# Performance work log

Measured on AMD Instinct MI355X. Metric: run time of the kernel, lower is better.

## Reference

```python
import jax, jax.numpy as jnp
import numpy as np

L = 14  # max_relative_position
H = 12  # num_heads
HD = 64  # head_dim


def rel_pos_embed(N, table_v, table_h):
    # 2D relative-position embedding with a leading CLS token (index 0).
    n = N - 1
    s = int(n ** 0.5)  # grid side (14)
    r = jnp.arange(n)
    dv = r[None, :] // s - r[:, None] // s  # vertical distance
    dh = r[None, :] % s - r[:, None] % s   # horizontal distance
    iv = jnp.clip(dv, -L, L) + L + 1
    ih = jnp.clip(dh, -L, L) + L + 1
    iv = jnp.pad(iv, ((1, 0), (1, 0)))  # CLS row/col -> index 0
    ih = jnp.pad(ih, ((1, 0), (1, 0)))
    return table_v[iv] + table_h[ih]  # [N, N, HD]


def setup_inputs() -> dict:
    key = jax.random.key(0)
    ks = jax.random.split(key, 11)
    B, N, E = 64, 197, 768
    T = 2 * L + 2  # rel-pos table rows (30)
    std = 0.02
    return {
        "x": jax.random.normal(ks[0], (B, N, E), jnp.float32),
        "wq": jax.random.normal(ks[1], (E, H * HD), jnp.float32) * std,
        "wk": jax.random.normal(ks[2], (E, H * HD), jnp.float32) * std,
        "wv": jax.random.normal(ks[3], (E, H * HD), jnp.float32) * std,
        "wproj": jax.random.normal(ks[4], (H * HD, E), jnp.float32) * std,
        "bproj": jnp.zeros((E,), jnp.float32),
        "rk_v": jax.random.normal(ks[5], (T, HD), jnp.float32) * std,
        "rk_h": jax.random.normal(ks[6], (T, HD), jnp.float32) * std,
        "rv_v": jax.random.normal(ks[7], (T, HD), jnp.float32) * std,
        "rv_h": jax.random.normal(ks[8], (T, HD), jnp.float32) * std,
    }


def reference(x, wq, wk, wv, wproj, bproj, rk_v, rk_h, rv_v, rv_h):
    B, N, E = x.shape
    scale = HD ** -0.5
    q = (x @ wq).reshape(B, N, H, HD).transpose(0, 2, 1, 3)  # [B,H,N,HD]
    k = (x @ wk).reshape(B, N, H, HD).transpose(0, 2, 1, 3)
    v = (x @ wv).reshape(B, N, H, HD).transpose(0, 2, 1, 3)

    attn = jnp.einsum('bhid,bhjd->bhij', q, k) * scale
    rpk = rel_pos_embed(N, rk_v, rk_h)  # [N,N,HD]
    attn = attn + jnp.einsum('bhid,ijd->bhij', q, rpk) * scale
    attn = jax.nn.softmax(attn, axis=-1)

    out = jnp.einsum('bhij,bhjd->bhid', attn, v)
    rpv = rel_pos_embed(N, rv_v, rv_h)
    out = out + jnp.einsum('bhij,ijd->bhid', attn, rpv)

    out = out.transpose(0, 2, 1, 3).reshape(B, N, H * HD)
    return out @ wproj + bproj
```

## Files before the change

### kernel.cpp

```cpp
#include <hip/hip_runtime.h>
#include <math.h>

typedef _Float16 f16;
typedef __attribute__((ext_vector_type(8))) _Float16 f16x8;
typedef __attribute__((ext_vector_type(4))) _Float16 f16x4;
typedef __attribute__((ext_vector_type(4))) float f32x4;

#define NH 12
#define HDIM 64
#define NTOK 197
#define EDIM 768
#define NB 64
#define MROWS (NB*NTOK)

__device__ __forceinline__ void wfence() {
    asm volatile("s_waitcnt lgkmcnt(0)" ::: "memory");
    __builtin_amdgcn_sched_barrier(0);
    __builtin_amdgcn_wave_barrier();
}

__device__ __forceinline__ unsigned div14(unsigned n) { return (n * 4682u) >> 16; }

__device__ __forceinline__ void gload16(const f16* g, f16* lds_base) {
    __builtin_amdgcn_global_load_lds(
        (const __attribute__((address_space(1))) void*)g,
        (__attribute__((address_space(3))) void*)lds_base, 16, 0, 0);
}

__global__ __launch_bounds__(256) void convert_x(
    const float* __restrict__ x, f16* __restrict__ xh)
{
    int idx = blockIdx.x * 256 + threadIdx.x;
    const float4* s = (const float4*)x + (size_t)idx * 2;
    float4 a = s[0], b = s[1];
    f16x8 h;
    h[0]=(f16)a.x; h[1]=(f16)a.y; h[2]=(f16)a.z; h[3]=(f16)a.w;
    h[4]=(f16)b.x; h[5]=(f16)b.y; h[6]=(f16)b.z; h[7]=(f16)b.w;
    *(f16x8*)(xh + (size_t)idx * 8) = h;
}

__global__ __launch_bounds__(256) void transpose_w(
    const float* __restrict__ wq, const float* __restrict__ wk,
    const float* __restrict__ wv, const float* __restrict__ wp,
    f16* __restrict__ wqkvT, f16* __restrict__ wpT)
{
    __shared__ float T[64][65];
    int m = blockIdx.z;
    const float* src = (m==0)?wq:(m==1)?wk:(m==2)?wv:wp;
    int k0 = blockIdx.x * 64, n0 = blockIdx.y * 64;
    int cidx = threadIdx.x & 63, r4 = threadIdx.x >> 6;
#pragma unroll
    for (int rr = 0; rr < 16; ++rr) {
        int kl = rr*4 + r4;
        T[kl][cidx] = src[(size_t)(k0+kl)*EDIM + n0 + cidx];
    }
    __syncthreads();
    f16* dst = (m < 3) ? (wqkvT + (size_t)m*EDIM*EDIM) : wpT;
#pragma unroll
    for (int rr = 0; rr < 16; ++rr) {
        int nl = rr*4 + r4;
        dst[(size_t)(n0+nl)*EDIM + k0 + cidx] = (f16)T[cidx][nl];
    }
}

__global__ __launch_bounds__(256) void prep_static(
    const float* __restrict__ rkv, const float* __restrict__ rkh,
    f16* __restrict__ gA, f16* __restrict__ gt_buf)
{
    int t = blockIdx.x * 256 + threadIdx.x;
    int stride = gridDim.x * 256;
    for (int i = t; i < 272*104; i += stride) {
        int row = i / 104, c = i - row*104;
        f16 v = (f16)0.f;
        if (c < 64) {
            if (row >= 208 && row < 238)      v = (f16)rkv[(row-208)*64 + c];
            else if (row >= 240 && row < 270) v = (f16)rkh[(row-240)*64 + c];
        } else if (c < 96 && row < 208) {
            int g = c - 64;
            if (row == 0) { if (g == 14 || g == 30) v = (f16)1.f; }
            else if (row <= 196) {
                int rm = row - 1;
                int gv = (int)div14((unsigned)rm), gh = rm - gv*14;
                if (g == gv || g == 16 + gh) v = (f16)1.f;
            }
        }
        gA[i] = v;
    }
    for (int i = t; i < 32*232; i += stride) {
        int g = i / 232, j = i - g*232;
        f16 v = (f16)0.f;
        if (j >= 1 && j <= 196) {
            int jm = j - 1;
            int gv = (int)div14((unsigned)jm), gh = jm - gv*14;
            if ((g < 14 && gv == g) || (g >= 16 && g < 30 && gh == g - 16))
                v = (f16)1.f;
        }
        gt_buf[i] = v;
    }
}

__global__ __launch_bounds__(512, 2) void gemm256(
    const f16* __restrict__ A, const f16* __restrict__ Bt,
    f16* __restrict__ q_o, f16* __restrict__ k_o, f16* __restrict__ v_o,
    float* __restrict__ p_o, const float* __restrict__ bias, int mode, int nxb)
{
    __shared__ f16 lds[4*16384];

    const int tid = threadIdx.x;
    const int l = tid & 63, w = tid >> 6;
    const int lr = l & 15, lq = l >> 4;
    const int wr = w >> 2, wc = w & 3;

    const int nwg = gridDim.x, orig = blockIdx.x;
    const int xcd = orig & 7, qc = nwg >> 3, rc = nwg & 7;
    const int wgid = (xcd < rc ? xcd*(qc+1) : rc*(qc+1) + (xcd-rc)*qc) + (orig >> 3);
    const int mband = wgid / nxb, nband = wgid - mband*nxb;
    const int m0 = mband << 8, n0 = nband << 8;

    const int scol = (((tid & 7) ^ ((tid >> 3) & 7)) << 3);
    const f16* aG[4]; const f16* bG[4];
#pragma unroll
    for (int p = 0; p < 4; ++p) {
        int rt = p*64 + (tid >> 3);
        int ra = m0 + rt; if (ra >= MROWS) ra = MROWS - 1;
        aG[p] = A  + (size_t)ra * EDIM + scol;
        bG[p] = Bt + (size_t)(n0 + rt) * EDIM + scol;
    }
    const int lbase = w * 512;

    f32x4 acc[8][4];
#pragma unroll
    for (int mt = 0; mt < 8; ++mt)
#pragma unroll
        for (int nt = 0; nt < 4; ++nt) {
            acc[mt][nt][0]=0.f; acc[mt][nt][1]=0.f;
            acc[mt][nt][2]=0.f; acc[mt][nt][3]=0.f;
        }

#pragma unroll
    for (int p = 0; p < 4; ++p) {
        gload16(aG[p], &lds[p*4096 + lbase]);
        gload16(bG[p], &lds[32768 + p*4096 + lbase]);
    }
    asm volatile("s_waitcnt vmcnt(0)" ::: "memory");
    __builtin_amdgcn_sched_barrier(0);
    __builtin_amdgcn_s_barrier();

    const int swz = (lr & 7) << 3;
    int cur = 0;
    for (int kt = 0; kt < 12; ++kt) {
        if (kt < 11) {
            const int ko = (kt + 1) * 64;
            const int nb = (cur ^ 1) * 16384;
#pragma unroll
            for (int p = 0; p < 4; ++p) {
                gload16(aG[p] + ko, &lds[nb + p*4096 + lbase]);
                gload16(bG[p] + ko, &lds[32768 + nb + p*4096 + lbase]);
            }
        }
        __builtin_amdgcn_sched_barrier(0);
        const f16* Ab = &lds[cur * 16384];
        const f16* Bb = &lds[32768 + cur * 16384];
#pragma unroll
        for (int ks = 0; ks < 2; ++ks) {
            const int kb = (ks*32 + lq*8) ^ swz;
            f16x8 bf[4];
#pragma unroll
            for (int nt = 0; nt < 4; ++nt)
                bf[nt] = *(const f16x8*)&Bb[(wc*64 + nt*16 + lr)*64 + kb];
#pragma unroll
            for (int mt = 0; mt < 8; ++mt) {
                f16x8 af = *(const f16x8*)&Ab[(wr*128 + mt*16 + lr)*64 + kb];
#pragma unroll
                for (int nt = 0; nt < 4; ++nt)
                    acc[mt][nt] = __builtin_amdgcn_mfma_f32_16x16x32_f16(
                        af, bf[nt], acc[mt][nt], 0, 0, 0);
            }
        }
        asm volatile("s_waitcnt vmcnt(0)" ::: "memory");
        __builtin_amdgcn_sched_barrier(0);
        __builtin_amdgcn_s_barrier();
        cur ^= 1;
    }

    if (mode == 0) {
        const int mat   = n0 / EDIM;
        const int hbase = ((n0 % EDIM) >> 6) + wc;
        f16* dst = (mat == 0) ? q_o : (mat == 1) ? k_o : v_o;
        f16* scr = &lds[w * 2304];
#pragma unroll
        for (int mt2 = 0; mt2 < 4; ++mt2) {
#pragma unroll
            for (int mtp = 0; mtp < 2; ++mtp) {
                const int mt = mt2*2 + mtp;
#pragma unroll
                for (int nt = 0; nt < 4; ++nt)
#pragma unroll
                    for (int rg = 0; rg < 4; ++rg)
                        scr[(mtp*16 + lq*4 + rg)*72 + nt*16 + lr] = (f16)acc[mt][nt][rg];
            }
            wfence();
#pragma unroll
            for (int i = 0; i < 4; ++i) {
                int row = (l >> 3) + i*8;
                f16x8 v = *(const f16x8*)&scr[row*72 + (l & 7)*8];
                int R = m0 + wr*128 + mt2*32 + row;
                if (R < MROWS) {
                    int bb = R / NTOK, nn = R - bb*NTOK;
                    *(f16x8*)&dst[((size_t)(bb*NH + hbase)*NTOK + nn)*HDIM + (l & 7)*8] = v;
                }
            }
            wfence();
        }
    } else {
#pragma unroll
        for (int mt = 0; mt < 8; ++mt)
#pragma unroll
            for (int rg = 0; rg < 4; ++rg) {
                int R = m0 + wr*128 + mt*16 + lq*4 + rg;
                if (R < MROWS) {
                    float* base = p_o + (size_t)R * EDIM + n0 + wc*64;
#pragma unroll
                    for (int nt = 0; nt < 4; ++nt) {
                        int c = nt*16 + lr;
                        base[c] = acc[mt][nt][rg] + bias[n0 + wc*64 + c];
                    }
                }
            }
    }
}

#define SKE 104
#define SVT 320
#define SGT 232
#define SWS 72
#define ATHR 832

__global__ __launch_bounds__(ATHR, 1) void attn_mfma(
    const f16* __restrict__ q_ws, const f16* __restrict__ k_ws,
    const f16* __restrict__ v_ws,
    const float* __restrict__ rvv, const float* __restrict__ rvh,
    const f16* __restrict__ gA, const f16* __restrict__ gt_buf,
    f16* __restrict__ o_ws)
{
    __shared__ f16 Kle[272*SKE];
    __shared__ f16 Vt[64*SVT];
    __shared__ f16 Gt[32*SGT];
    __shared__ f16 WSh[13*16*SWS];

    const int tid = threadIdx.x;
    const int w = tid >> 6, l = tid & 63;
    const int lr = l & 15, lq = l >> 4;
    const int bh = blockIdx.x;
    const int b = bh / NH, h = bh - b * NH;
    const f16* Qp = q_ws + (size_t)bh * NTOK * HDIM;
    const f16* Kp = k_ws + (size_t)bh * NTOK * HDIM;
    const f16* Vp = v_ws + (size_t)bh * NTOK * HDIM;
    f16* wsh = &WSh[w * 16 * SWS];

    for (int idx = tid; idx < 197*8; idx += ATHR) {
        int row = idx >> 3, c8 = (idx & 7) << 3;
        *(f16x8*)&Kle[row*SKE + c8] = *(const f16x8*)(Kp + row*64 + c8);
    }
    for (int idx = tid; idx < 197*5; idx += ATHR) {
        int row = idx / 5, c = idx - row*5;
        int off = row*SKE + 64 + c*8;
        *(f16x8*)&Kle[off] = *(const f16x8*)(gA + off);
    }
    for (int idx = tid; idx < 75*13; idx += ATHR) {
        int off = 197*SKE + idx*8;
        *(f16x8*)&Kle[off] = *(const f16x8*)(gA + off);
    }
    for (int idx = tid; idx < 32*29; idx += ATHR) {
        int off = idx*8;
        *(f16x8*)&Gt[off] = *(const f16x8*)(gt_buf + off);
    }
    for (int idx = tid; idx < 8*SVT; idx += ATHR) {
        int dlow = idx & 7, k = idx >> 3;
        int kx = k ^ (dlow << 3);
        bool isV = (k < NTOK), isA = (k >= 208 && k < 238), isB = (k >= 238 && k < 268);
#pragma unroll
        for (int e = 0; e < 8; ++e) {
            int d = (e << 3) + dlow;
            f16 val = (f16)0.f;
            if (isV)      val = Vp[k*64 + d];
            else if (isA) val = (f16)rvv[(k-208)*64 + d];
            else if (isB) val = (f16)rvh[(k-238)*64 + d];
            Vt[d*SVT + kx] = val;
        }
    }
    __syncthreads();

    const int src0 = ((l >> 4) & 1) * 32 + lr;
    const int src1 = src0 + 16;

    {
        const int tt = w;
        const int i0 = tt * 16;
        const int iq = i0 + lr;
        const int iqc = (iq > 196) ? 196 : iq;
        const f16* qsrc = Qp + iqc*64 + lq*8;
        f16x8 qf0 = *(const f16x8*)qsrc;
        f16x8 qf1 = *(const f16x8*)(qsrc + 32);

        __builtin_amdgcn_s_setprio(1);
        f32x4 pacc[4];
#pragma unroll
        for (int ct = 0; ct < 4; ++ct) {
            f32x4 a; a[0]=0.f; a[1]=0.f; a[2]=0.f; a[3]=0.f;
            const int krow = (13+ct)*16 + lr;
            f16x8 kf0 = *(f16x8*)&Kle[krow*SKE + lq*8];
            f16x8 kf1 = *(f16x8*)&Kle[krow*SKE + 32 + lq*8];
            a = __builtin_amdgcn_mfma_f32_16x16x32_f16(kf0, qf0, a, 0, 0, 0);
            a = __builtin_amdgcn_mfma_f32_16x16x32_f16(kf1, qf1, a, 0, 0, 0);
            pacc[ct] = a;
        }
        __builtin_amdgcn_s_setprio(0);
#pragma unroll
        for (int ct = 0; ct < 4; ++ct)
#pragma unroll
            for (int rg = 0; rg < 4; ++rg)
                wsh[lr*SWS + ct*16 + lq*4 + rg] = (f16)pacc[ct][rg];
        wfence();

        int id_ = 0, ih_ = 0;
        const bool qcls = (iq == 0);
        if (iq > 0) { unsigned v = div14((unsigned)(iq-1)); id_ = (int)v; ih_ = (iq-1) - (int)v*14; }
        f16x8 qcf;
#pragma unroll
        for (int e = 0; e < 8; ++e) {
            int g = lq*8 + e;
            int toff;
            if (g < 14)       toff = qcls ? 0 : (g - id_ + 15);
            else if (g == 14) toff = 0;
            else if (g == 15) toff = 63;
            else if (g < 30)  toff = qcls ? 32 : (32 + (g-16) - ih_ + 15);
            else if (g == 30) toff = 32;
            else              toff = 63;
            qcf[e] = wsh[lr*SWS + toff];
        }

        f32x4 acc[13];
        __builtin_amdgcn_s_setprio(1);
#pragma unroll
        for (int ct = 0; ct < 13; ++ct) {
            f32x4 a; a[0]=0.f; a[1]=0.f; a[2]=0.f; a[3]=0.f;
            const int krow = ct*16 + lr;
            f16x8 kf0 = *(f16x8*)&Kle[krow*SKE + lq*8];
            f16x8 kf1 = *(f16x8*)&Kle[krow*SKE + 32 + lq*8];
            f16x8 gf  = *(f16x8*)&Kle[krow*SKE + 64 + lq*8];
            a = __builtin_amdgcn_mfma_f32_16x16x32_f16(kf0, qf0, a, 0, 0, 0);
            a = __builtin_amdgcn_mfma_f32_16x16x32_f16(kf1, qf1, a, 0, 0, 0);
            a = __builtin_amdgcn_mfma_f32_16x16x32_f16(gf,  qcf, a, 0, 0, 0);
            acc[ct] = a;
        }
        __builtin_amdgcn_s_setprio(0);

#pragma unroll
        for (int rg = 0; rg < 4; ++rg)
            if (lq*4 + rg > 4) acc[12][rg] = -1e30f;

        float m = -1e30f;
#pragma unroll
        for (int ct = 0; ct < 13; ++ct)
#pragma unroll
            for (int rg = 0; rg < 4; ++rg) m = fmaxf(m, acc[ct][rg]);
        m = fmaxf(m, __shfl_xor(m, 16));
        m = fmaxf(m, __shfl_xor(m, 32));
        const float C1 = 0.125f * 1.44269504088896f;
        const float nm = -m * C1;
        float ssum = 0.f;
#pragma unroll
        for (int ct = 0; ct < 13; ++ct)
#pragma unroll
            for (int rg = 0; rg < 4; ++rg) {
                float p = exp2f(fmaf(acc[ct][rg], C1, nm));
                acc[ct][rg] = p; ssum += p;
            }
        ssum += __shfl_xor(ssum, 16);
        ssum += __shfl_xor(ssum, 32);
        const float inv = 1.f / ssum;
        const float pn00 = acc[0][0] * inv;

        unsigned pk[13][2];
#pragma unroll
        for (int ct = 0; ct < 13; ++ct) {
            union { f16x4 hh; unsigned u[2]; } t;
            t.hh[0] = (f16)(acc[ct][0] * inv);
            t.hh[1] = (f16)(acc[ct][1] * inv);
            t.hh[2] = (f16)(acc[ct][2] * inv);
            t.hh[3] = (f16)(acc[ct][3] * inv);
            pk[ct][0] = t.u[0]; pk[ct][1] = t.u[1];
        }

        f16x8 pa[7];
#pragma unroll
        for (int kc = 0; kc < 7; ++kc) {
            const int ctA = 2*kc;
            const int ctB = (kc == 6) ? 12 : 2*kc + 1;
            unsigned A0 = (unsigned)__shfl((int)pk[ctA][0], src0);
            unsigned A1 = (unsigned)__shfl((int)pk[ctA][1], src0);
            unsigned A2 = (unsigned)__shfl((int)pk[ctA][0], src1);
            unsigned A3 = (unsigned)__shfl((int)pk[ctA][1], src1);
            unsigned B0 = (unsigned)__shfl((int)pk[ctB][0], src0);
            unsigned B1 = (unsigned)__shfl((int)pk[ctB][1], src0);
            unsigned B2 = (unsigned)__shfl((int)pk[ctB][0], src1);
            unsigned B3 = (unsigned)__shfl((int)pk[ctB][1], src1);
            bool hiHalf = (lq >= 2);
            union { unsigned u[4]; f16x8 v; } f;
            f.u[0] = hiHalf ? B0 : A0;
            f.u[1] = hiHalf ? B1 : A1;
            f.u[2] = hiHalf ? B2 : A2;
            f.u[3] = hiHalf ? B3 : A3;
            if (kc == 6 && hiHalf) { f.u[0]=0; f.u[1]=0; f.u[2]=0; f.u[3]=0; }
            pa[kc] = f.v;
        }

        f32x4 gacc[2];
#pragma unroll
        for (int ct = 0; ct < 2; ++ct) { gacc[ct][0]=0.f; gacc[ct][1]=0.f; gacc[ct][2]=0.f; gacc[ct][3]=0.f; }
        __builtin_amdgcn_s_setprio(1);
#pragma unroll
        for (int kc = 0; kc < 7; ++kc) {
#pragma unroll
            for (int ct = 0; ct < 2; ++ct) {
                f16x8 gf = *(f16x8*)&Gt[(ct*16 + lr)*SGT + kc*32 + lq*8];
                gacc[ct] = __builtin_amdgcn_mfma_f32_16x16x32_f16(pa[kc], gf, gacc[ct], 0, 0, 0);
            }
        }
        __builtin_amdgcn_s_setprio(0);

#pragma unroll
        for (int z = 0; z < 2; ++z) {
            int zi = z*64 + l;
            int zr = zi >> 3, zc = (zi & 7) << 3;
            f16x8 zz;
#pragma unroll
            for (int e = 0; e < 8; ++e) zz[e] = (f16)0.f;
            *(f16x8*)&wsh[zr*SWS + zc] = zz;
        }
        wfence();
#pragma unroll
        for (int rg = 0; rg < 4; ++rg) {
            int il = lq*4 + rg;
            int is_ = i0 + il;
            if (lr < 14 && is_ > 0) {
                unsigned v = div14((unsigned)(is_-1));
                int id2 = (int)v, ih2 = (is_-1) - (int)v*14;
                wsh[il*SWS + (lr - id2 + 15)]      = (f16)gacc[0][rg];
                wsh[il*SWS + 30 + (lr - ih2 + 15)] = (f16)gacc[1][rg];
            }
        }
        if (lq == 0 && !(i0 == 0 && lr == 0)) {
            wsh[lr*SWS + 0]  = (f16)pn00;
            wsh[lr*SWS + 30] = (f16)pn00;
        }
        if (i0 == 0) {
            float sv = (lq == 0) ? gacc[0][0] : 0.f;
            float sh = (lq == 0) ? gacc[1][0] : 0.f;
            sv += __shfl_xor(sv, 1); sv += __shfl_xor(sv, 2);
            sv += __shfl_xor(sv, 4); sv += __shfl_xor(sv, 8);
            sh += __shfl_xor(sh, 1); sh += __shfl_xor(sh, 2);
            sh += __shfl_xor(sh, 4); sh += __shfl_xor(sh, 8);
            if (l == 0) {
                wsh[0]  = (f16)(sv + pn00);
                wsh[30] = (f16)(sh + pn00);
            }
        }
        wfence();

        f16x8 sfr[2];
#pragma unroll
        for (int kc2 = 0; kc2 < 2; ++kc2)
            sfr[kc2] = *(f16x8*)&wsh[lr*SWS + kc2*32 + lq*8];

        f32x4 oacc[4];
#pragma unroll
        for (int ct = 0; ct < 4; ++ct) { oacc[ct][0]=0.f; oacc[ct][1]=0.f; oacc[ct][2]=0.f; oacc[ct][3]=0.f; }
        __builtin_amdgcn_s_setprio(1);
        const int swz = (lr & 7) << 3;
#pragma unroll
        for (int kc = 0; kc < 7; ++kc) {
#pragma unroll
            for (int ct = 0; ct < 4; ++ct) {
                f16x8 vf = *(f16x8*)&Vt[(ct*16 + lr)*SVT + ((kc*32 + lq*8) ^ swz)];
                oacc[ct] = __builtin_amdgcn_mfma_f32_16x16x32_f16(pa[kc], vf, oacc[ct], 0, 0, 0);
            }
        }
#pragma unroll
        for (int kc2 = 0; kc2 < 2; ++kc2) {
#pragma unroll
            for (int ct = 0; ct < 4; ++ct) {
                f16x8 vf = *(f16x8*)&Vt[(ct*16 + lr)*SVT + ((208 + kc2*32 + lq*8) ^ swz)];
                oacc[ct] = __builtin_amdgcn_mfma_f32_16x16x32_f16(sfr[kc2], vf, oacc[ct], 0, 0, 0);
            }
        }
        __builtin_amdgcn_s_setprio(0);

#pragma unroll
        for (int ct = 0; ct < 4; ++ct)
#pragma unroll
            for (int rg = 0; rg < 4; ++rg) {
                int io = i0 + lq*4 + rg;
                if (io < NTOK) {
                    int d = ct*16 + lr;
                    o_ws[((size_t)(b * NTOK + io) * NH + h) * HDIM + d] = (f16)oacc[ct][rg];
                }
            }
    }
}

extern "C" void kernel_launch(void* const* d_in, const int* in_sizes, int n_in,
                              void* d_out, int out_size, void* d_ws, size_t ws_size,
                              hipStream_t stream)
{
    const float* x     = (const float*)d_in[0];
    const float* wq    = (const float*)d_in[1];
    const float* wk    = (const float*)d_in[2];
    const float* wv    = (const float*)d_in[3];
    const float* wproj = (const float*)d_in[4];
    const float* bproj = (const float*)d_in[5];
    const float* rkv   = (const float*)d_in[6];
    const float* rkh   = (const float*)d_in[7];
    const float* rvv   = (const float*)d_in[8];
    const float* rvh   = (const float*)d_in[9];

    f16* ws = (f16*)d_ws;
    const size_t sz = (size_t)MROWS * EDIM;
    f16* xh    = ws;
    f16* qh    = xh + sz;
    f16* kh    = qh + sz;
    f16* vh    = kh + sz;
    f16* oh    = vh + sz;
    f16* wqkvT = oh + sz;
    f16* wpT   = wqkvT + (size_t)3*EDIM*EDIM;
    f16* gA    = wpT   + (size_t)EDIM*EDIM;
    f16* gtb   = gA    + 272*104;

    convert_x  <<<4728, 256, 0, stream>>>(x, xh);
    transpose_w<<<dim3(12, 12, 4), 256, 0, stream>>>(wq, wk, wv, wproj, wqkvT, wpT);
    prep_static<<<32, 256, 0, stream>>>(rkv, rkh, gA, gtb);
    gemm256    <<<50*9, 512, 0, stream>>>(xh, wqkvT, qh, kh, vh,
                                          nullptr, nullptr, 0, 9);
    attn_mfma  <<<NB * NH, ATHR, 0, stream>>>(qh, kh, vh,
                                              rvv, rvh, gA, gtb, oh);
    gemm256    <<<50*3, 512, 0, stream>>>(oh, wpT, nullptr, nullptr, nullptr,
                                          (float*)d_out, bproj, 1, 3);
}
```

Before: 152.7 us.

## Fuse prep kernels into one launch and XOR-swizzle attention LDS tiles

Merges the three preprocessing kernels (x conversion, weight transpose, static table build) into a single launch that dispatches on block index, removing two kernel launches. It also widens the K/extra-table and Gt LDS row strides to power-of-two sizes and applies an XOR swizzle to column offsets so MFMA fragment reads avoid LDS bank conflicts. The static tables are written pre-swizzled in global memory so the attention kernel can copy them in one uniform loop. This uses more LDS per block and adds index arithmetic on every fragment load.

```diff
diff --git a/kernel.cpp b/kernel.cpp
--- a/kernel.cpp
+++ b/kernel.cpp
@@ -27,75 +27,75 @@
         (__attribute__((address_space(3))) void*)lds_base, 16, 0, 0);
 }
 
-__global__ __launch_bounds__(256) void convert_x(
-    const float* __restrict__ x, f16* __restrict__ xh)
-{
-    int idx = blockIdx.x * 256 + threadIdx.x;
-    const float4* s = (const float4*)x + (size_t)idx * 2;
-    float4 a = s[0], b = s[1];
-    f16x8 h;
-    h[0]=(f16)a.x; h[1]=(f16)a.y; h[2]=(f16)a.z; h[3]=(f16)a.w;
-    h[4]=(f16)b.x; h[5]=(f16)b.y; h[6]=(f16)b.z; h[7]=(f16)b.w;
-    *(f16x8*)(xh + (size_t)idx * 8) = h;
-}
-
-__global__ __launch_bounds__(256) void transpose_w(
+__global__ __launch_bounds__(256) void prep_all(
+    const float* __restrict__ x,
     const float* __restrict__ wq, const float* __restrict__ wk,
     const float* __restrict__ wv, const float* __restrict__ wp,
-    f16* __restrict__ wqkvT, f16* __restrict__ wpT)
+    const float* __restrict__ rkv, const float* __restrict__ rkh,
+    f16* __restrict__ xh, f16* __restrict__ wqkvT, f16* __restrict__ wpT,
+    f16* __restrict__ gA, f16* __restrict__ gt_buf)
 {
     __shared__ float T[64][65];
-    int m = blockIdx.z;
-    const float* src = (m==0)?wq:(m==1)?wk:(m==2)?wv:wp;
-    int k0 = blockIdx.x * 64, n0 = blockIdx.y * 64;
-    int cidx = threadIdx.x & 63, r4 = threadIdx.x >> 6;
-#pragma unroll
-    for (int rr = 0; rr < 16; ++rr) {
-        int kl = rr*4 + r4;
-        T[kl][cidx] = src[(size_t)(k0+kl)*EDIM + n0 + cidx];
-    }
-    __syncthreads();
-    f16* dst = (m < 3) ? (wqkvT + (size_t)m*EDIM*EDIM) : wpT;
-#pragma unroll
-    for (int rr = 0; rr < 16; ++rr) {
-        int nl = rr*4 + r4;
-        dst[(size_t)(n0+nl)*EDIM + k0 + cidx] = (f16)T[cidx][nl];
-    }
-}
-
-__global__ __launch_bounds__(256) void prep_static(
-    const float* __restrict__ rkv, const float* __restrict__ rkh,
-    f16* __restrict__ gA, f16* __restrict__ gt_buf)
-{
-    int t = blockIdx.x * 256 + threadIdx.x;
-    int stride = gridDim.x * 256;
-    for (int i = t; i < 272*104; i += stride) {
-        int row = i / 104, c = i - row*104;
-        f16 v = (f16)0.f;
-        if (c < 64) {
-            if (row >= 208 && row < 238)      v = (f16)rkv[(row-208)*64 + c];
-            else if (row >= 240 && row < 270) v = (f16)rkh[(row-240)*64 + c];
-        } else if (c < 96 && row < 208) {
-            int g = c - 64;
-            if (row == 0) { if (g == 14 || g == 30) v = (f16)1.f; }
-            else if (row <= 196) {
-                int rm = row - 1;
-                int gv = (int)div14((unsigned)rm), gh = rm - gv*14;
-                if (g == gv || g == 16 + gh) v = (f16)1.f;
-            }
-        }
-        gA[i] = v;
-    }
-    for (int i = t; i < 32*232; i += stride) {
-        int g = i / 232, j = i - g*232;
-        f16 v = (f16)0.f;
-        if (j >= 1 && j <= 196) {
-            int jm = j - 1;
-            int gv = (int)div14((unsigned)jm), gh = jm - gv*14;
-            if ((g < 14 && gv == g) || (g >= 16 && g < 30 && gh == g - 16))
-                v = (f16)1.f;
-        }
-        gt_buf[i] = v;
+    const int bid = blockIdx.x;
+    if (bid < 4728) {
+        int idx = bid * 256 + threadIdx.x;
+        const float4* s = (const float4*)x + (size_t)idx * 2;
+        float4 a = s[0], b = s[1];
+        f16x8 h;
+        h[0]=(f16)a.x; h[1]=(f16)a.y; h[2]=(f16)a.z; h[3]=(f16)a.w;
+        h[4]=(f16)b.x; h[5]=(f16)b.y; h[6]=(f16)b.z; h[7]=(f16)b.w;
+        *(f16x8*)(xh + (size_t)idx * 8) = h;
+    } else if (bid < 5304) {
+        int b2 = bid - 4728;
+        int m = b2 / 144, rem = b2 - m*144;
+        const float* src = (m==0)?wq:(m==1)?wk:(m==2)?wv:wp;
+        int k0 = (rem / 12) * 64, n0 = (rem % 12) * 64;
+        int cidx = threadIdx.x & 63, r4 = threadIdx.x >> 6;
+#pragma unroll
+        for (int rr = 0; rr < 16; ++rr) {
+            int kl = rr*4 + r4;
+            T[kl][cidx] = src[(size_t)(k0+kl)*EDIM + n0 + cidx];
+        }
+        __syncthreads();
+        f16* dst = (m < 3) ? (wqkvT + (size_t)m*EDIM*EDIM) : wpT;
+#pragma unroll
+        for (int rr = 0; rr < 16; ++rr) {
+            int nl = rr*4 + r4;
+            dst[(size_t)(n0+nl)*EDIM + k0 + cidx] = (f16)T[cidx][nl];
+        }
+    } else {
+        int t = (bid - 5304) * 256 + threadIdx.x;
+        const int stride = 32 * 256;
+        for (int i = t; i < 272*128; i += stride) {
+            int row = i >> 7, cs = i & 127;
+            int c = cs ^ ((row & 7) << 3);
+            f16 v = (f16)0.f;
+            if (c < 64) {
+                if (row >= 208 && row < 238)      v = (f16)rkv[(row-208)*64 + c];
+                else if (row >= 240 && row < 270) v = (f16)rkh[(row-240)*64 + c];
+            } else if (c < 96 && row < 208) {
+                int g = c - 64;
+                if (row == 0) { if (g == 14 || g == 30) v = (f16)1.f; }
+                else if (row <= 196) {
+                    int rm = row - 1;
+                    int gv = (int)div14((unsigned)rm), gh = rm - gv*14;
+                    if (g == gv || g == 16 + gh) v = (f16)1.f;
+                }
+            }
+            gA[i] = v;
+        }
+        for (int i = t; i < 32*256; i += stride) {
+            int g = i >> 8, cs = i & 255;
+            int j = cs ^ ((g & 7) << 3);
+            f16 v = (f16)0.f;
+            if (j >= 1 && j <= 196) {
+                int jm = j - 1;
+                int gv = (int)div14((unsigned)jm), gh = jm - gv*14;
+                if ((g < 14 && gv == g) || (g >= 16 && g < 30 && gh == g - 16))
+                    v = (f16)1.f;
+            }
+            gt_buf[i] = v;
+        }
     }
 }
 
@@ -230,9 +230,9 @@
     }
 }
 
-#define SKE 104
+#define SKE 128
 #define SVT 320
-#define SGT 232
+#define SGT 256
 #define SWS 72
 #define ATHR 832
 
@@ -258,21 +258,19 @@
     const f16* Vp = v_ws + (size_t)bh * NTOK * HDIM;
     f16* wsh = &WSh[w * 16 * SWS];
 
-    for (int idx = tid; idx < 197*8; idx += ATHR) {
-        int row = idx >> 3, c8 = (idx & 7) << 3;
-        *(f16x8*)&Kle[row*SKE + c8] = *(const f16x8*)(Kp + row*64 + c8);
-    }
-    for (int idx = tid; idx < 197*5; idx += ATHR) {
-        int row = idx / 5, c = idx - row*5;
-        int off = row*SKE + 64 + c*8;
-        *(f16x8*)&Kle[off] = *(const f16x8*)(gA + off);
-    }
-    for (int idx = tid; idx < 75*13; idx += ATHR) {
-        int off = 197*SKE + idx*8;
-        *(f16x8*)&Kle[off] = *(const f16x8*)(gA + off);
-    }
-    for (int idx = tid; idx < 32*29; idx += ATHR) {
-        int off = idx*8;
+    for (int idx = tid; idx < 272*16; idx += ATHR) {
+        int row = idx >> 4, cs8 = (idx & 15) << 3;
+        f16x8 v;
+        if (row < NTOK && cs8 < 64) {
+            int c8 = cs8 ^ ((row & 7) << 3);
+            v = *(const f16x8*)(Kp + row*64 + c8);
+        } else {
+            v = *(const f16x8*)(gA + row*SKE + cs8);
+        }
+        *(f16x8*)&Kle[row*SKE + cs8] = v;
+    }
+    for (int idx = tid; idx < 32*32; idx += ATHR) {
+        int off = idx * 8;
         *(f16x8*)&Gt[off] = *(const f16x8*)(gt_buf + off);
     }
     for (int idx = tid; idx < 8*SVT; idx += ATHR) {
@@ -303,14 +301,16 @@
         f16x8 qf0 = *(const f16x8*)qsrc;
         f16x8 qf1 = *(const f16x8*)(qsrc + 32);
 
+        const int sw = (lr & 7) << 3;
+
         __builtin_amdgcn_s_setprio(1);
         f32x4 pacc[4];
 #pragma unroll
         for (int ct = 0; ct < 4; ++ct) {
             f32x4 a; a[0]=0.f; a[1]=0.f; a[2]=0.f; a[3]=0.f;
             const int krow = (13+ct)*16 + lr;
-            f16x8 kf0 = *(f16x8*)&Kle[krow*SKE + lq*8];
-            f16x8 kf1 = *(f16x8*)&Kle[krow*SKE + 32 + lq*8];
+            f16x8 kf0 = *(f16x8*)&Kle[krow*SKE + ((lq*8) ^ sw)];
+            f16x8 kf1 = *(f16x8*)&Kle[krow*SKE + ((32 + lq*8) ^ sw)];
             a = __builtin_amdgcn_mfma_f32_16x16x32_f16(kf0, qf0, a, 0, 0, 0);
             a = __builtin_amdgcn_mfma_f32_16x16x32_f16(kf1, qf1, a, 0, 0, 0);
             pacc[ct] = a;
@@ -346,9 +346,9 @@
         for (int ct = 0; ct < 13; ++ct) {
             f32x4 a; a[0]=0.f; a[1]=0.f; a[2]=0.f; a[3]=0.f;
             const int krow = ct*16 + lr;
-            f16x8 kf0 = *(f16x8*)&Kle[krow*SKE + lq*8];
-            f16x8 kf1 = *(f16x8*)&Kle[krow*SKE + 32 + lq*8];
-            f16x8 gf  = *(f16x8*)&Kle[krow*SKE + 64 + lq*8];
+            f16x8 kf0 = *(f16x8*)&Kle[krow*SKE + ((lq*8) ^ sw)];
+            f16x8 kf1 = *(f16x8*)&Kle[krow*SKE + ((32 + lq*8) ^ sw)];
+            f16x8 gf  = *(f16x8*)&Kle[krow*SKE + ((64 + lq*8) ^ sw)];
             a = __builtin_amdgcn_mfma_f32_16x16x32_f16(kf0, qf0, a, 0, 0, 0);
             a = __builtin_amdgcn_mfma_f32_16x16x32_f16(kf1, qf1, a, 0, 0, 0);
             a = __builtin_amdgcn_mfma_f32_16x16x32_f16(gf,  qcf, a, 0, 0, 0);
@@ -424,7 +424,7 @@
         for (int kc = 0; kc < 7; ++kc) {
 #pragma unroll
             for (int ct = 0; ct < 2; ++ct) {
-                f16x8 gf = *(f16x8*)&Gt[(ct*16 + lr)*SGT + kc*32 + lq*8];
+                f16x8 gf = *(f16x8*)&Gt[(ct*16 + lr)*SGT + ((kc*32 + lq*8) ^ sw)];
                 gacc[ct] = __builtin_amdgcn_mfma_f32_16x16x32_f16(pa[kc], gf, gacc[ct], 0, 0, 0);
             }
         }
@@ -478,12 +478,11 @@
 #pragma unroll
         for (int ct = 0; ct < 4; ++ct) { oacc[ct][0]=0.f; oacc[ct][1]=0.f; oacc[ct][2]=0.f; oacc[ct][3]=0.f; }
         __builtin_amdgcn_s_setprio(1);
-        const int swz = (lr & 7) << 3;
 #pragma unroll
         for (int kc = 0; kc < 7; ++kc) {
 #pragma unroll
             for (int ct = 0; ct < 4; ++ct) {
-                f16x8 vf = *(f16x8*)&Vt[(ct*16 + lr)*SVT + ((kc*32 + lq*8) ^ swz)];
+                f16x8 vf = *(f16x8*)&Vt[(ct*16 + lr)*SVT + ((kc*32 + lq*8) ^ sw)];
                 oacc[ct] = __builtin_amdgcn_mfma_f32_16x16x32_f16(pa[kc], vf, oacc[ct], 0, 0, 0);
             }
         }
@@ -491,7 +490,7 @@
         for (int kc2 = 0; kc2 < 2; ++kc2) {
 #pragma unroll
             for (int ct = 0; ct < 4; ++ct) {
-                f16x8 vf = *(f16x8*)&Vt[(ct*16 + lr)*SVT + ((208 + kc2*32 + lq*8) ^ swz)];
+                f16x8 vf = *(f16x8*)&Vt[(ct*16 + lr)*SVT + ((208 + kc2*32 + lq*8) ^ sw)];
                 oacc[ct] = __builtin_amdgcn_mfma_f32_16x16x32_f16(sfr[kc2], vf, oacc[ct], 0, 0, 0);
             }
         }
@@ -535,15 +534,14 @@
     f16* wqkvT = oh + sz;
     f16* wpT   = wqkvT + (size_t)3*EDIM*EDIM;
     f16* gA    = wpT   + (size_t)EDIM*EDIM;
-    f16* gtb   = gA    + 272*104;
-
-    convert_x  <<<4728, 256, 0, stream>>>(x, xh);
-    transpose_w<<<dim3(12, 12, 4), 256, 0, stream>>>(wq, wk, wv, wproj, wqkvT, wpT);
-    prep_static<<<32, 256, 0, stream>>>(rkv, rkh, gA, gtb);
-    gemm256    <<<50*9, 512, 0, stream>>>(xh, wqkvT, qh, kh, vh,
-                                          nullptr, nullptr, 0, 9);
-    attn_mfma  <<<NB * NH, ATHR, 0, stream>>>(qh, kh, vh,
-                                              rvv, rvh, gA, gtb, oh);
-    gemm256    <<<50*3, 512, 0, stream>>>(oh, wpT, nullptr, nullptr, nullptr,
-                                          (float*)d_out, bproj, 1, 3);
+    f16* gtb   = gA    + 272*128;
+
+    prep_all<<<5336, 256, 0, stream>>>(x, wq, wk, wv, wproj, rkv, rkh,
+                                       xh, wqkvT, wpT, gA, gtb);
+    gemm256 <<<50*9, 512, 0, stream>>>(xh, wqkvT, qh, kh, vh,
+                                       nullptr, nullptr, 0, 9);
+    attn_mfma<<<NB * NH, ATHR, 0, stream>>>(qh, kh, vh,
+                                            rvv, rvh, gA, gtb, oh);
+    gemm256 <<<50*3, 512, 0, stream>>>(oh, wpT, nullptr, nullptr, nullptr,
+                                       (float*)d_out, bproj, 1, 3);
 }
```

New measurement: 148.1 us. 3.0% less time.
